# Kernel optimization log

Measured on AMD Instinct MI355X. Metric: run time of the kernel, lower is better.

Reference implementation:

```python
import jax, jax.numpy as jnp
import numpy as np

EPS = 1e-8

def l2norm(x, axis=-1):
    norm = jnp.sqrt(jnp.sum(x * x, axis=axis, keepdims=True)) + EPS
    return x / norm

def setup_inputs() -> dict:
    key = jax.random.key(0)
    ks = jax.random.split(key, 4)
    B, Lq, Ls, d, sim_dim = 128, 128, 256, 1024, 256
    query = jax.random.normal(ks[0], (B, Lq, d), dtype=jnp.float32)
    context = jax.random.normal(ks[1], (B, Ls, d), dtype=jnp.float32)
    matrix = jax.random.uniform(ks[2], (B, Lq, d), dtype=jnp.float32)
    W = jax.random.normal(ks[3], (sim_dim, d), dtype=jnp.float32) * (1.0 / np.sqrt(d))
    b = jnp.zeros((sim_dim,), dtype=jnp.float32)
    smooth = 9
    return {"query": query, "context": context, "matrix": matrix, "W": W, "b": b, "smooth": smooth}

def reference(query, context, matrix, W, b, smooth):
    # cross_attention
    q = query * matrix                                   # (B, Lq, d)
    attn = jnp.einsum('bsd,bqd->bsq', context, q)        # (B, Ls, Lq)
    attn = jnp.where(attn >= 0, attn, 0.1 * attn)        # LeakyReLU(0.1)
    attn = l2norm(attn, axis=-1)                         # normalize over Lq
    attn = jnp.swapaxes(attn, 1, 2)                      # (B, Lq, Ls)
    attn = jax.nn.softmax(attn * smooth, axis=2)         # softmax over source
    wcontext = jnp.einsum('bqs,bsd->bqd', attn, context) # (B, Lq, d)
    wcontext = l2norm(wcontext, axis=-1)
    # alignment vector
    sim_rep = (query - wcontext) ** 2                    # (B, Lq, d)
    sim_rep = jnp.einsum('bqd,kd->bqk', sim_rep, W) + b  # Linear d -> sim_dim
    sim_rep = l2norm(sim_rep, axis=-1)
    return sim_rep
```

## Files before the change

### kernel.cpp

```cpp
#include <hip/hip_runtime.h>
#include <hip/hip_bf16.h>

constexpr int B  = 128;
constexpr int LQ = 128;
constexpr int LS = 256;
constexpr int D  = 1024;
constexpr int SD = 256;
constexpr float EPS = 1e-8f;

typedef __attribute__((ext_vector_type(8))) __bf16 bf16x8;
typedef __attribute__((ext_vector_type(4))) float f32x4;

__device__ inline ushort f2bf(float f) {
    union { float f; uint u; } v{f};
    uint r = v.u + 0x7fffu + ((v.u >> 16) & 1u);
    return (ushort)(r >> 16);
}
__device__ inline float bf2f(ushort u) {
    union { uint u; float f; } v{(uint)u << 16};
    return v.f;
}
__device__ inline uint4 pack8(float4 a, float4 b) {
    union { ushort us[8]; uint4 u4; } r;
    r.us[0]=f2bf(a.x); r.us[1]=f2bf(a.y); r.us[2]=f2bf(a.z); r.us[3]=f2bf(a.w);
    r.us[4]=f2bf(b.x); r.us[5]=f2bf(b.y); r.us[6]=f2bf(b.z); r.us[7]=f2bf(b.w);
    return r.u4;
}
__device__ inline int swz(int row, int kbyte) {
    return row * 128 + (kbyte ^ ((row & 7) << 4));
}
__device__ inline bf16x8 lds_frag(const ushort* base, int row, int kk, int lane) {
    int kbyte = kk * 64 + (lane >> 4) * 16;
    return *(const bf16x8*)((const char*)base + swz(row, kbyte));
}
__device__ inline int swz512(int row, int kbyte) {
    return row * 512 + (kbyte ^ ((row & 7) << 4));
}
__device__ inline f32x4 mfma16(bf16x8 a, bf16x8 b, f32x4 c) {
    return __builtin_amdgcn_mfma_f32_16x16x32_bf16(a, b, c, 0, 0, 0);
}

__global__ __launch_bounds__(256) void wconv_kernel(
    const float* __restrict__ W, ushort* __restrict__ Wb)
{
    size_t i = ((size_t)blockIdx.x * 256 + threadIdx.x) * 8;
    float4 a = *(const float4*)(W + i);
    float4 b = *(const float4*)(W + i + 4);
    *(uint4*)(Wb + i) = pack8(a, b);
}

__global__ __launch_bounds__(512, 2) void gemmA_kernel(
    const float* __restrict__ query, const float* __restrict__ mat,
    const float* __restrict__ ctx, const int* __restrict__ smooth_p,
    ushort* __restrict__ E)
{
    const int bid = blockIdx.x;
    const int xcd = bid & 7, idx = bid >> 3;
    const int b  = xcd * 16 + (idx >> 1);
    const int sh = idx & 1;
    const int n0 = sh * 128;
    __shared__ ushort SH[4][128 * 64];
    __shared__ float colssP[2][128];
    __shared__ float invsm[128];
    ushort* Et = &SH[0][0];

    const int t = threadIdx.x;
    const int wv = t >> 6, l = t & 63;
    const int wq = wv >> 2, wsv = wv & 3;

    const float* Qb = query + (size_t)b * LQ * D;
    const float* Mb = mat   + (size_t)b * LQ * D;
    const float* Cb = ctx   + ((size_t)b * LS + n0) * D;
    const int r0 = t >> 3, k8 = (t & 7) * 8;

    f32x4 acc[4][2] = {};
    float4 q0,q1,q2,q3, m0,m1,m2,m3, c0,c1,c2,c3;

    auto loadT = [&](int k0) {
        const float* qp = Qb + (size_t)r0 * D + k0 + k8;
        const float* mp = Mb + (size_t)r0 * D + k0 + k8;
        q0 = *(const float4*)qp; q1 = *(const float4*)(qp + 4);
        m0 = *(const float4*)mp; m1 = *(const float4*)(mp + 4);
        qp += (size_t)64 * D;  mp += (size_t)64 * D;
        q2 = *(const float4*)qp; q3 = *(const float4*)(qp + 4);
        m2 = *(const float4*)mp; m3 = *(const float4*)(mp + 4);
        const float* cp = Cb + (size_t)r0 * D + k0 + k8;
        c0 = *(const float4*)cp; c1 = *(const float4*)(cp + 4);
        cp += (size_t)64 * D;
        c2 = *(const float4*)cp; c3 = *(const float4*)(cp + 4);
    };
    auto storeT = [&](int buf) {
        float4 p1{q0.x*m0.x, q0.y*m0.y, q0.z*m0.z, q0.w*m0.w};
        float4 p2{q1.x*m1.x, q1.y*m1.y, q1.z*m1.z, q1.w*m1.w};
        *(uint4*)((char*)&SH[buf][0] + swz(r0, k8 * 2)) = pack8(p1, p2);
        float4 p3{q2.x*m2.x, q2.y*m2.y, q2.z*m2.z, q2.w*m2.w};
        float4 p4{q3.x*m3.x, q3.y*m3.y, q3.z*m3.z, q3.w*m3.w};
        *(uint4*)((char*)&SH[buf][0] + swz(r0 + 64, k8 * 2)) = pack8(p3, p4);
        *(uint4*)((char*)&SH[2 + buf][0] + swz(r0, k8 * 2))      = pack8(c0, c1);
        *(uint4*)((char*)&SH[2 + buf][0] + swz(r0 + 64, k8 * 2)) = pack8(c2, c3);
    };
    auto mfmaT = [&](int buf) {
#pragma unroll
        for (int kk = 0; kk < 2; ++kk) {
            bf16x8 bfr0 = lds_frag(&SH[2 + buf][0], wsv * 32 + (l & 15), kk, l);
            bf16x8 bfr1 = lds_frag(&SH[2 + buf][0], wsv * 32 + 16 + (l & 15), kk, l);
#pragma unroll
            for (int i = 0; i < 4; ++i) {
                bf16x8 af = lds_frag(&SH[buf][0], wq * 64 + i * 16 + (l & 15), kk, l);
                acc[i][0] = mfma16(af, bfr0, acc[i][0]);
                acc[i][1] = mfma16(af, bfr1, acc[i][1]);
            }
        }
    };

    const int ks0 = ((bid >> 1) * 5) & 15;

    loadT(ks0 * 64);
    storeT(0);
    __syncthreads();
    int cur = 0;
#pragma unroll 1
    for (int ks = 0; ks < 15; ++ks) {
        loadT((((ks0 + ks + 1) & 15)) * 64);
        mfmaT(cur);
        storeT(cur ^ 1);
        __syncthreads();
        cur ^= 1;
    }
    mfmaT(cur);

#pragma unroll
    for (int n = 0; n < 2; ++n) {
        float csum = 0.f;
#pragma unroll
        for (int i = 0; i < 4; ++i)
#pragma unroll
            for (int r = 0; r < 4; ++r) {
                float v = acc[i][n][r];
                v = v >= 0.f ? v : 0.1f * v;
                acc[i][n][r] = v;
                csum += v * v;
            }
        csum += __shfl_xor(csum, 16);
        csum += __shfl_xor(csum, 32);
        if (l < 16) colssP[wq][wsv * 32 + n * 16 + l] = csum;
    }
    __syncthreads();
    const float sm = (float)(*smooth_p);
    if (t < 128) invsm[t] = sm / (sqrtf(colssP[0][t] + colssP[1][t]) + EPS);
    __syncthreads();
#pragma unroll
    for (int n = 0; n < 2; ++n) {
        const float invc = invsm[wsv * 32 + n * 16 + (l & 15)];
#pragma unroll
        for (int i = 0; i < 4; ++i)
#pragma unroll
            for (int r = 0; r < 4; ++r) {
                int row = wq * 64 + i * 16 + (l >> 4) * 4 + r;
                Et[row * 136 + wsv * 32 + n * 16 + (l & 15)] =
                    f2bf(__expf(acc[i][n][r] * invc));
            }
    }
    __syncthreads();
    ushort* Eg = E + (size_t)b * LQ * LS + n0;
#pragma unroll
    for (int j = 0; j < 4; ++j) {
        int c = t + j * 512;
        int row = c >> 4, s8 = (c & 15) * 8;
        *(uint4*)(Eg + (size_t)row * LS + s8) = *(const uint4*)(Et + row * 136 + s8);
    }
}

__global__ __launch_bounds__(512, 2) void pv_kernel(
    const ushort* __restrict__ E, const float* __restrict__ ctx,
    ushort* __restrict__ wctx, float* __restrict__ rowssP)
{
    const int bid = blockIdx.x;
    const int xcd = bid & 7, idx = bid >> 3;
    const int b  = xcd * 16 + (idx >> 1);
    const int dh = idx & 1;
    const int dglob0 = dh * 512;

    __shared__ ushort Es[128 * 256];
    __shared__ ushort Bs[64 * 264];
    __shared__ float rsumL[128];
    __shared__ float rinv[128];
    __shared__ float rowssL[128][4];

    const int t = threadIdx.x;
    const int wv = t >> 6, l = t & 63;
    const int wq = wv >> 2, wd = wv & 3;

    const ushort* Eb = E + (size_t)b * LQ * LS;
    const int cc = t & 31, rr = t >> 5;
    float part[8];
#pragma unroll
    for (int p = 0; p < 8; ++p) {
        int row = rr + p * 16;
        uint4 v = *(const uint4*)(Eb + (size_t)row * LS + cc * 8);
        *(uint4*)((char*)Es + swz512(row, cc * 16)) = v;
        const ushort* us = (const ushort*)&v;
        float s = 0.f;
#pragma unroll
        for (int j = 0; j < 8; ++j) s += bf2f(us[j]);
        part[p] = s;
    }
    rowssL[t >> 2][t & 3] = 0.f;
#pragma unroll
    for (int p = 0; p < 8; ++p) {
        float s = part[p];
        s += __shfl_xor(s, 1);  s += __shfl_xor(s, 2);
        s += __shfl_xor(s, 4);  s += __shfl_xor(s, 8);
        s += __shfl_xor(s, 16);
        if ((l & 31) == 0) rsumL[rr + p * 16] = s;
    }

    const float* Cb = ctx + (size_t)b * LS * D + dglob0;
    const int sr = t >> 4, c4 = (t & 15) * 4;
    float4 cr[8];
#pragma unroll
    for (int p = 0; p < 8; ++p)
        cr[p] = *(const float4*)(Cb + (size_t)(p * 32 + sr) * D + c4);

    __syncthreads();
    if (t < 128) rinv[t] = 1.0f / rsumL[t];

#pragma unroll
    for (int p = 0; p < 8; ++p) {
        int s = p * 32 + sr;
        Bs[(c4 + 0) * 264 + s] = f2bf(cr[p].x);
        Bs[(c4 + 1) * 264 + s] = f2bf(cr[p].y);
        Bs[(c4 + 2) * 264 + s] = f2bf(cr[p].z);
        Bs[(c4 + 3) * 264 + s] = f2bf(cr[p].w);
    }
    __syncthreads();

    ushort* Ob = wctx + (size_t)b * LQ * D + dglob0;

#pragma unroll 1
    for (int dt = 0; dt < 8; ++dt) {
        if (dt < 7) {
#pragma unroll
            for (int p = 0; p < 8; ++p)
                cr[p] = *(const float4*)(Cb + (size_t)(p * 32 + sr) * D + (dt + 1) * 64 + c4);
        }
        f32x4 acc[4] = {};
#pragma unroll
        for (int kk = 0; kk < 8; ++kk) {
            const ushort* bp = Bs + (wd * 16 + (l & 15)) * 264 + kk * 32 + (l >> 4) * 8;
            bf16x8 bfr = *(const bf16x8*)bp;
#pragma unroll
            for (int i = 0; i < 4; ++i) {
                bf16x8 af = *(const bf16x8*)((const char*)Es +
                    swz512(wq * 64 + i * 16 + (l & 15), kk * 64 + (l >> 4) * 16));
                acc[i] = mfma16(af, bfr, acc[i]);
            }
        }
#pragma unroll
        for (int i = 0; i < 4; ++i)
#pragma unroll
            for (int r = 0; r < 4; ++r) {
                int row = wq * 64 + i * 16 + (l >> 4) * 4 + r;
                float wval = acc[i][r] * rinv[row];
                float p2 = wval * wval;
                p2 += __shfl_xor(p2, 1); p2 += __shfl_xor(p2, 2);
                p2 += __shfl_xor(p2, 4); p2 += __shfl_xor(p2, 8);
                if ((l & 15) == 0) rowssL[row][wd] += p2;
                Ob[(size_t)row * D + dt * 64 + wd * 16 + (l & 15)] = f2bf(wval);
            }
        __syncthreads();
        if (dt < 7) {
#pragma unroll
            for (int p = 0; p < 8; ++p) {
                int s = p * 32 + sr;
                Bs[(c4 + 0) * 264 + s] = f2bf(cr[p].x);
                Bs[(c4 + 1) * 264 + s] = f2bf(cr[p].y);
                Bs[(c4 + 2) * 264 + s] = f2bf(cr[p].z);
                Bs[(c4 + 3) * 264 + s] = f2bf(cr[p].w);
            }
            __syncthreads();
        }
    }
    if (t < 128)
        rowssP[(size_t)b * 256 + dh * 128 + t] =
            rowssL[t][0] + rowssL[t][1] + rowssL[t][2] + rowssL[t][3];
}

__global__ __launch_bounds__(512, 2) void gemm3_kernel(
    const ushort* __restrict__ wctx, const float* __restrict__ query,
    const float* __restrict__ rowssP, const ushort* __restrict__ Wb,
    const float* __restrict__ bias, float* __restrict__ out)
{
    const int m0 = blockIdx.x * 64;
    const int b  = blockIdx.y;
    __shared__ ushort As[64 * 64];
    __shared__ ushort Bs[256 * 64];
    __shared__ float red[64][4];
    __shared__ float invr[64];
    const int t = threadIdx.x;
    const int w = t >> 6, l = t & 63;
    const int wm = (w >> 2) * 32, wn = (w & 3) * 64;

    const int arow = t >> 3, ako = (t & 7) * 8;
    const float r0v = rowssP[(size_t)b * 256 + m0 + arow];
    const float r1v = rowssP[(size_t)b * 256 + 128 + m0 + arow];
    const float ivq = 1.0f / (sqrtf(r0v + r1v) + EPS);
    const float* Qp  = query + ((size_t)b * LQ + m0 + arow) * D + ako;
    const ushort* Wp = wctx  + ((size_t)b * LQ + m0 + arow) * D + ako;

    f32x4 acc[2][4] = {};

    for (int k0 = 0; k0 < D; k0 += 64) {
        if (k0) __syncthreads();
        {
            uint4 wu = *(const uint4*)(Wp + k0);
            float4 q1 = *(const float4*)(Qp + k0);
            float4 q2 = *(const float4*)(Qp + k0 + 4);
            float d0 = q1.x - bf2f((ushort)(wu.x & 0xffff)) * ivq;
            float d1 = q1.y - bf2f((ushort)(wu.x >> 16))    * ivq;
            float d2 = q1.z - bf2f((ushort)(wu.y & 0xffff)) * ivq;
            float d3 = q1.w - bf2f((ushort)(wu.y >> 16))    * ivq;
            float d4 = q2.x - bf2f((ushort)(wu.z & 0xffff)) * ivq;
            float d5 = q2.y - bf2f((ushort)(wu.z >> 16))    * ivq;
            float d6 = q2.z - bf2f((ushort)(wu.w & 0xffff)) * ivq;
            float d7 = q2.w - bf2f((ushort)(wu.w >> 16))    * ivq;
            float4 s1{d0*d0, d1*d1, d2*d2, d3*d3};
            float4 s2{d4*d4, d5*d5, d6*d6, d7*d7};
            *(uint4*)((char*)As + swz(arow, ako * 2)) = pack8(s1, s2);
        }
#pragma unroll
        for (int j = 0; j < 4; ++j) {
            int c = t + j * 512;
            int row = c >> 3, ko = (c & 7) * 8;
            *(uint4*)((char*)Bs + swz(row, ko * 2)) =
                *(const uint4*)(Wb + (size_t)row * D + k0 + ko);
        }
        __syncthreads();
#pragma unroll
        for (int kk = 0; kk < 2; ++kk) {
            bf16x8 af[2], bfr[4];
#pragma unroll
            for (int i = 0; i < 2; ++i) af[i] = lds_frag(As, wm + i * 16 + (l & 15), kk, l);
#pragma unroll
            for (int n = 0; n < 4; ++n) bfr[n] = lds_frag(Bs, wn + n * 16 + (l & 15), kk, l);
#pragma unroll
            for (int i = 0; i < 2; ++i)
#pragma unroll
                for (int n = 0; n < 4; ++n) acc[i][n] = mfma16(af[i], bfr[n], acc[i][n]);
        }
    }
#pragma unroll
    for (int n = 0; n < 4; ++n) {
        float bv = bias[wn + n * 16 + (l & 15)];
#pragma unroll
        for (int i = 0; i < 2; ++i)
#pragma unroll
            for (int r = 0; r < 4; ++r) acc[i][n][r] += bv;
    }
#pragma unroll
    for (int i = 0; i < 2; ++i)
#pragma unroll
        for (int r = 0; r < 4; ++r) {
            float p = 0.f;
#pragma unroll
            for (int n = 0; n < 4; ++n) p += acc[i][n][r] * acc[i][n][r];
#pragma unroll
            for (int off = 1; off < 16; off <<= 1) p += __shfl_xor(p, off);
            int rowl = wm + i * 16 + (l >> 4) * 4 + r;
            if ((l & 15) == 0) red[rowl][w & 3] = p;
        }
    __syncthreads();
    if (t < 64) {
        float s = red[t][0] + red[t][1] + red[t][2] + red[t][3];
        invr[t] = 1.0f / (sqrtf(s) + EPS);
    }
    __syncthreads();
    float* Ob = out + ((size_t)b * LQ + m0) * SD;
#pragma unroll
    for (int i = 0; i < 2; ++i)
#pragma unroll
        for (int r = 0; r < 4; ++r) {
            int rowl = wm + i * 16 + (l >> 4) * 4 + r;
            float iv = invr[rowl];
#pragma unroll
            for (int n = 0; n < 4; ++n) {
                int col = wn + n * 16 + (l & 15);
                Ob[(size_t)rowl * SD + col] = acc[i][n][r] * iv;
            }
        }
}

extern "C" void kernel_launch(void* const* d_in, const int* in_sizes, int n_in,
                              void* d_out, int out_size, void* d_ws, size_t ws_size,
                              hipStream_t stream)
{
    const float* query  = (const float*)d_in[0];
    const float* ctx    = (const float*)d_in[1];
    const float* mat    = (const float*)d_in[2];
    const float* W      = (const float*)d_in[3];
    const float* bias   = (const float*)d_in[4];
    const int*   smooth = (const int*)d_in[5];
    float* out = (float*)d_out;

    char* ws = (char*)d_ws;
    ushort* wctx   = (ushort*)ws;
    ushort* E      = (ushort*)(ws + (size_t)32 * 1024 * 1024);
    ushort* Wb     = (ushort*)(ws + (size_t)40 * 1024 * 1024);
    float*  rowssP = (float*)(ws + (size_t)(40 * 1024 + 512) * 1024);

    wconv_kernel<<<dim3(SD * D / (256 * 8)), 256, 0, stream>>>(W, Wb);
    gemmA_kernel<<<dim3(256), 512, 0, stream>>>(query, mat, ctx, smooth, E);
    pv_kernel<<<dim3(256), 512, 0, stream>>>(E, ctx, wctx, rowssP);
    gemm3_kernel<<<dim3(2, B), 512, 0, stream>>>(wctx, query, rowssP, Wb, bias, out);
}
```

Baseline: 160.8 us.

## Pre-pack query*matrix and context into bf16 tiled layouts before GEMMs

Adds two elementwise pack kernels that compute query*matrix and convert context to bf16, each stored in contiguous 64-column tile blocks. gemmA and pv_kernel then read these compact bf16 tiles instead of fp32 rows, which halves the bytes read from context in both kernels and makes gemmA's loads fully contiguous. The cost is an extra pass that reads all fp32 inputs and writes the bf16 copies, plus extra launches and a larger workspace. The staggered k-start in gemmA is removed.

```diff
diff --git a/kernel.cpp b/kernel.cpp
--- a/kernel.cpp
+++ b/kernel.cpp
@@ -49,10 +49,40 @@
     *(uint4*)(Wb + i) = pack8(a, b);
 }
 
+__global__ __launch_bounds__(256) void qmpack_kernel(
+    const float* __restrict__ query, const float* __restrict__ mat,
+    ushort* __restrict__ qmt)
+{
+    size_t i8 = ((size_t)blockIdx.x * 256 + threadIdx.x) * 8;
+    float4 q1 = *(const float4*)(query + i8), q2 = *(const float4*)(query + i8 + 4);
+    float4 m1 = *(const float4*)(mat + i8),   m2 = *(const float4*)(mat + i8 + 4);
+    float4 p1{q1.x*m1.x, q1.y*m1.y, q1.z*m1.z, q1.w*m1.w};
+    float4 p2{q2.x*m2.x, q2.y*m2.y, q2.z*m2.z, q2.w*m2.w};
+    const int b  = (int)(i8 >> 17);
+    const int rem = (int)(i8 & 131071);
+    const int r  = rem >> 10;
+    const int k  = rem & 1023;
+    const int kt = k >> 6, kc = k & 63;
+    *(uint4*)(qmt + ((size_t)(b * 16 + kt) * 8192 + r * 64 + kc)) = pack8(p1, p2);
+}
+
+__global__ __launch_bounds__(256) void cpack_kernel(
+    const float* __restrict__ ctx, ushort* __restrict__ ctxt)
+{
+    size_t i8 = ((size_t)blockIdx.x * 256 + threadIdx.x) * 8;
+    float4 c1 = *(const float4*)(ctx + i8), c2 = *(const float4*)(ctx + i8 + 4);
+    const int b  = (int)(i8 >> 18);
+    const int rem = (int)(i8 & 262143);
+    const int s  = rem >> 10;
+    const int k  = rem & 1023;
+    const int sh = s >> 7, sr = s & 127;
+    const int kt = k >> 6, kc = k & 63;
+    *(uint4*)(ctxt + ((size_t)((b * 2 + sh) * 16 + kt) * 8192 + sr * 64 + kc)) = pack8(c1, c2);
+}
+
 __global__ __launch_bounds__(512, 2) void gemmA_kernel(
-    const float* __restrict__ query, const float* __restrict__ mat,
-    const float* __restrict__ ctx, const int* __restrict__ smooth_p,
-    ushort* __restrict__ E)
+    const ushort* __restrict__ qmt, const ushort* __restrict__ ctxt,
+    const int* __restrict__ smooth_p, ushort* __restrict__ E)
 {
     const int bid = blockIdx.x;
     const int xcd = bid & 7, idx = bid >> 3;
@@ -68,36 +98,28 @@
     const int wv = t >> 6, l = t & 63;
     const int wq = wv >> 2, wsv = wv & 3;
 
-    const float* Qb = query + (size_t)b * LQ * D;
-    const float* Mb = mat   + (size_t)b * LQ * D;
-    const float* Cb = ctx   + ((size_t)b * LS + n0) * D;
-    const int r0 = t >> 3, k8 = (t & 7) * 8;
+    const ushort* Ab = qmt  + (size_t)b * 16 * 8192;
+    const ushort* Bb = ctxt + (size_t)(b * 2 + sh) * 16 * 8192;
+
+    const int ra = t >> 3,        ka = (t & 7) * 8;
+    const int rb = (t >> 3) + 64, kb = (t & 7) * 8;
 
     f32x4 acc[4][2] = {};
-    float4 q0,q1,q2,q3, m0,m1,m2,m3, c0,c1,c2,c3;
-
-    auto loadT = [&](int k0) {
-        const float* qp = Qb + (size_t)r0 * D + k0 + k8;
-        const float* mp = Mb + (size_t)r0 * D + k0 + k8;
-        q0 = *(const float4*)qp; q1 = *(const float4*)(qp + 4);
-        m0 = *(const float4*)mp; m1 = *(const float4*)(mp + 4);
-        qp += (size_t)64 * D;  mp += (size_t)64 * D;
-        q2 = *(const float4*)qp; q3 = *(const float4*)(qp + 4);
-        m2 = *(const float4*)mp; m3 = *(const float4*)(mp + 4);
-        const float* cp = Cb + (size_t)r0 * D + k0 + k8;
-        c0 = *(const float4*)cp; c1 = *(const float4*)(cp + 4);
-        cp += (size_t)64 * D;
-        c2 = *(const float4*)cp; c3 = *(const float4*)(cp + 4);
+    uint4 a0, a1, b0, b1;
+
+    auto loadT = [&](int kt) {
+        const ushort* ap = Ab + (size_t)kt * 8192;
+        const ushort* bp = Bb + (size_t)kt * 8192;
+        a0 = *(const uint4*)(ap + t * 8);
+        a1 = *(const uint4*)(ap + (t + 512) * 8);
+        b0 = *(const uint4*)(bp + t * 8);
+        b1 = *(const uint4*)(bp + (t + 512) * 8);
     };
     auto storeT = [&](int buf) {
-        float4 p1{q0.x*m0.x, q0.y*m0.y, q0.z*m0.z, q0.w*m0.w};
-        float4 p2{q1.x*m1.x, q1.y*m1.y, q1.z*m1.z, q1.w*m1.w};
-        *(uint4*)((char*)&SH[buf][0] + swz(r0, k8 * 2)) = pack8(p1, p2);
-        float4 p3{q2.x*m2.x, q2.y*m2.y, q2.z*m2.z, q2.w*m2.w};
-        float4 p4{q3.x*m3.x, q3.y*m3.y, q3.z*m3.z, q3.w*m3.w};
-        *(uint4*)((char*)&SH[buf][0] + swz(r0 + 64, k8 * 2)) = pack8(p3, p4);
-        *(uint4*)((char*)&SH[2 + buf][0] + swz(r0, k8 * 2))      = pack8(c0, c1);
-        *(uint4*)((char*)&SH[2 + buf][0] + swz(r0 + 64, k8 * 2)) = pack8(c2, c3);
+        *(uint4*)((char*)&SH[buf][0] + swz(ra, ka * 2))     = a0;
+        *(uint4*)((char*)&SH[buf][0] + swz(rb, kb * 2))     = a1;
+        *(uint4*)((char*)&SH[2 + buf][0] + swz(ra, ka * 2)) = b0;
+        *(uint4*)((char*)&SH[2 + buf][0] + swz(rb, kb * 2)) = b1;
     };
     auto mfmaT = [&](int buf) {
 #pragma unroll
@@ -113,15 +135,13 @@
         }
     };
 
-    const int ks0 = ((bid >> 1) * 5) & 15;
-
-    loadT(ks0 * 64);
+    loadT(0);
     storeT(0);
     __syncthreads();
     int cur = 0;
 #pragma unroll 1
     for (int ks = 0; ks < 15; ++ks) {
-        loadT((((ks0 + ks + 1) & 15)) * 64);
+        loadT(ks + 1);
         mfmaT(cur);
         storeT(cur ^ 1);
         __syncthreads();
@@ -172,7 +192,7 @@
 }
 
 __global__ __launch_bounds__(512, 2) void pv_kernel(
-    const ushort* __restrict__ E, const float* __restrict__ ctx,
+    const ushort* __restrict__ E, const ushort* __restrict__ ctxt,
     ushort* __restrict__ wctx, float* __restrict__ rowssP)
 {
     const int bid = blockIdx.x;
@@ -215,12 +235,17 @@
         if ((l & 31) == 0) rsumL[rr + p * 16] = s;
     }
 
-    const float* Cb = ctx + (size_t)b * LS * D + dglob0;
+    const ushort* Cb = ctxt + (size_t)b * 2 * 16 * 8192;
     const int sr = t >> 4, c4 = (t & 15) * 4;
-    float4 cr[8];
-#pragma unroll
-    for (int p = 0; p < 8; ++p)
-        cr[p] = *(const float4*)(Cb + (size_t)(p * 32 + sr) * D + c4);
+    auto csrc = [&](int dt, int p) {
+        int S = p * 32 + sr;
+        int sh2 = S >> 7, r2 = S & 127;
+        int kt = dh * 8 + dt;
+        return Cb + (size_t)(sh2 * 16 + kt) * 8192 + r2 * 64 + c4;
+    };
+    uint2 cr[8];
+#pragma unroll
+    for (int p = 0; p < 8; ++p) cr[p] = *(const uint2*)csrc(0, p);
 
     __syncthreads();
     if (t < 128) rinv[t] = 1.0f / rsumL[t];
@@ -228,10 +253,11 @@
 #pragma unroll
     for (int p = 0; p < 8; ++p) {
         int s = p * 32 + sr;
-        Bs[(c4 + 0) * 264 + s] = f2bf(cr[p].x);
-        Bs[(c4 + 1) * 264 + s] = f2bf(cr[p].y);
-        Bs[(c4 + 2) * 264 + s] = f2bf(cr[p].z);
-        Bs[(c4 + 3) * 264 + s] = f2bf(cr[p].w);
+        const ushort* us = (const ushort*)&cr[p];
+        Bs[(c4 + 0) * 264 + s] = us[0];
+        Bs[(c4 + 1) * 264 + s] = us[1];
+        Bs[(c4 + 2) * 264 + s] = us[2];
+        Bs[(c4 + 3) * 264 + s] = us[3];
     }
     __syncthreads();
 
@@ -241,8 +267,7 @@
     for (int dt = 0; dt < 8; ++dt) {
         if (dt < 7) {
 #pragma unroll
-            for (int p = 0; p < 8; ++p)
-                cr[p] = *(const float4*)(Cb + (size_t)(p * 32 + sr) * D + (dt + 1) * 64 + c4);
+            for (int p = 0; p < 8; ++p) cr[p] = *(const uint2*)csrc(dt + 1, p);
         }
         f32x4 acc[4] = {};
 #pragma unroll
@@ -273,10 +298,11 @@
 #pragma unroll
             for (int p = 0; p < 8; ++p) {
                 int s = p * 32 + sr;
-                Bs[(c4 + 0) * 264 + s] = f2bf(cr[p].x);
-                Bs[(c4 + 1) * 264 + s] = f2bf(cr[p].y);
-                Bs[(c4 + 2) * 264 + s] = f2bf(cr[p].z);
-                Bs[(c4 + 3) * 264 + s] = f2bf(cr[p].w);
+                const ushort* us = (const ushort*)&cr[p];
+                Bs[(c4 + 0) * 264 + s] = us[0];
+                Bs[(c4 + 1) * 264 + s] = us[1];
+                Bs[(c4 + 2) * 264 + s] = us[2];
+                Bs[(c4 + 3) * 264 + s] = us[3];
             }
             __syncthreads();
         }
@@ -403,13 +429,17 @@
     float* out = (float*)d_out;
 
     char* ws = (char*)d_ws;
-    ushort* wctx   = (ushort*)ws;
-    ushort* E      = (ushort*)(ws + (size_t)32 * 1024 * 1024);
-    ushort* Wb     = (ushort*)(ws + (size_t)40 * 1024 * 1024);
-    float*  rowssP = (float*)(ws + (size_t)(40 * 1024 + 512) * 1024);
+    ushort* ctxt   = (ushort*)ws;
+    ushort* qmt    = (ushort*)(ws + (size_t)64 * 1024 * 1024);
+    ushort* wctx   = qmt;
+    ushort* E      = (ushort*)(ws + (size_t)96 * 1024 * 1024);
+    ushort* Wb     = (ushort*)(ws + (size_t)104 * 1024 * 1024);
+    float*  rowssP = (float*)(ws + (size_t)(104 * 1024 + 512) * 1024);
 
     wconv_kernel<<<dim3(SD * D / (256 * 8)), 256, 0, stream>>>(W, Wb);
-    gemmA_kernel<<<dim3(256), 512, 0, stream>>>(query, mat, ctx, smooth, E);
-    pv_kernel<<<dim3(256), 512, 0, stream>>>(E, ctx, wctx, rowssP);
+    qmpack_kernel<<<dim3((size_t)B * LQ * D / (256 * 8)), 256, 0, stream>>>(query, mat, qmt);
+    cpack_kernel<<<dim3((size_t)B * LS * D / (256 * 8)), 256, 0, stream>>>(ctx, ctxt);
+    gemmA_kernel<<<dim3(256), 512, 0, stream>>>(qmt, ctxt, smooth, E);
+    pv_kernel<<<dim3(256), 512, 0, stream>>>(E, ctxt, wctx, rowssP);
     gemm3_kernel<<<dim3(2, B), 512, 0, stream>>>(wctx, query, rowssP, Wb, bias, out);
 }
```

New measurement: 177.0 us. 10.0% more time.
